# Optimization experiments

Measured on AMD Instinct MI355X. Metric: run time of the kernel, lower is better.

## Reference

```python
import jax, jax.numpy as jnp
import numpy as np

N_NODES = 100000
N_EDGES = 1600000
D_NODE = 32
D_EDGE = 16
D_HID = 64
D_OUT = 32


def setup_inputs() -> dict:
    key = jax.random.key(0)
    ks = jax.random.split(key, 7)
    x = jax.random.normal(ks[0], (N_NODES, D_NODE), dtype=jnp.float32)
    edge_index = jax.random.randint(ks[1], (2, N_EDGES), 0, N_NODES, dtype=jnp.int64)
    edge_attr = jax.random.normal(ks[2], (N_EDGES, D_EDGE), dtype=jnp.float32)
    # 2-layer MLP params (Linear -> ReLU -> Linear), He-ish scaling
    W1 = jax.random.normal(ks[3], (D_NODE + D_EDGE, D_HID), dtype=jnp.float32) * (2.0 / (D_NODE + D_EDGE)) ** 0.5
    b1 = jnp.zeros((D_HID,), dtype=jnp.float32)
    W2 = jax.random.normal(ks[4], (D_HID, D_OUT), dtype=jnp.float32) * (2.0 / D_HID) ** 0.5
    b2 = jnp.zeros((D_OUT,), dtype=jnp.float32)
    return {"x": x, "edge_index": edge_index, "edge_attr": edge_attr,
            "W1": W1, "b1": b1, "W2": W2, "b2": b2}


def reference(x, edge_index, edge_attr, W1, b1, W2, b2):
    row, col = edge_index[0], edge_index[1]
    # gather source-node feats and concat with edge feats: [E, d_node + d_edge]
    inp = jnp.concatenate([x[col], edge_attr], axis=1)
    # 2-layer MLP over edges
    h = jax.nn.relu(inp @ W1 + b1)
    messages = h @ W2 + b2  # [E, d_out]
    # scatter-sum aggregate by destination node
    message = jax.ops.segment_sum(messages, row, num_segments=x.shape[0])
    return message
```

## Files before the change

kernel.cpp:

```cpp
#include <hip/hip_runtime.h>
#include <hip/hip_bf16.h>
#include <stdint.h>

#define N_NODES 100000
#define N_EDGES 1600000
#define D_NODE  32
#define D_EDGE  16
#define D_IN    48
#define D_HID   64
#define D_OUT   32

#define NFLAGS_OFF  ((size_t)0)
#define NB1_OFF     ((size_t)64)
#define NB2_OFF     ((size_t)320)
#define W1BF_OFF    ((size_t)1024)
#define W2BF_OFF    ((size_t)9216)
#define COUNTS_OFF  ((size_t)65536)
#define OFFSETS_OFF ((size_t)466944)
#define BLKSUM_OFF  ((size_t)917504)
#define RANK_OFF    ((size_t)1048576)
#define MSG_OFF     ((size_t)8388608)

#define SCAN_NB 391

typedef __attribute__((ext_vector_type(8))) short bf16x8;
typedef __attribute__((ext_vector_type(4))) float f32x4;

__device__ inline float bf2f(unsigned int u16) {
    return __uint_as_float(u16 << 16);
}
__device__ inline unsigned short f2bf_rne(float f) {
    unsigned int x = __float_as_uint(f);
    unsigned int r = (x + 0x7FFFu + ((x >> 16) & 1u)) >> 16;
    return (unsigned short)r;
}
__device__ inline unsigned int pk_bf2(float a, float b) {
    float2 f; f.x = a; f.y = b;
    __hip_bfloat162 h = __float22bfloat162_rn(f);
    return *reinterpret_cast<unsigned int*>(&h);
}
__device__ inline float ld_f(const void* p, int i, int isbf) {
    if (isbf) return bf2f(((const unsigned short*)p)[i]);
    return ((const float*)p)[i];
}
__device__ inline bf16x8 pack_bf8(float4 v0, float4 v1) {
    union { unsigned int u[4]; bf16x8 v; } r;
    r.u[0] = pk_bf2(v0.x, v0.y);
    r.u[1] = pk_bf2(v0.z, v0.w);
    r.u[2] = pk_bf2(v1.x, v1.y);
    r.u[3] = pk_bf2(v1.z, v1.w);
    return r.v;
}

__global__ __launch_bounds__(256) void prep_kernel(
        const void* __restrict__ xq, const void* __restrict__ idxq,
        const void* __restrict__ W1q, const void* __restrict__ b1q,
        const void* __restrict__ W2q, const void* __restrict__ b2q,
        char* __restrict__ ws) {
    const int t = threadIdx.x;
    const int i0 = blockIdx.x * 256 + t;
    int* counts = (int*)(ws + COUNTS_OFF);
    if (i0 < N_NODES) counts[i0] = 0;
    if (blockIdx.x != 0) return;

    __shared__ int s_isbf;
    if (t < 64) {
        unsigned short u = ((const unsigned short*)xq)[t];
        unsigned long long mb = __ballot(((u >> 7) & 0xFF) >= 140);
        int wodd = ((const int*)idxq)[2 * t + 1];
        unsigned long long mi = __ballot(wodd != 0);
        if (t == 0) {
            int* flags = (int*)(ws + NFLAGS_OFF);
            flags[0] = (mb == 0ULL);
            flags[1] = (mi == 0ULL);
            s_isbf = (mb == 0ULL);
        }
    }
    __syncthreads();
    const int isbf = s_isbf;
    float* b1 = (float*)(ws + NB1_OFF);
    float* b2 = (float*)(ws + NB2_OFF);
    unsigned short* w1b = (unsigned short*)(ws + W1BF_OFF);
    unsigned short* w2b = (unsigned short*)(ws + W2BF_OFF);

    if (t < D_HID) b1[t] = ld_f(b1q, t, isbf);
    if (t < D_OUT) b2[t] = ld_f(b2q, t, isbf);

    for (int i = t; i < D_HID * 64; i += 256) {
        int n = i >> 6, k = i & 63;
        float v = (k < D_IN) ? ld_f(W1q, k * D_HID + n, isbf) : 0.0f;
        w1b[i] = f2bf_rne(v);
    }
    for (int i = t; i < D_OUT * 64; i += 256) {
        int n = i >> 6, k = i & 63;
        w2b[i] = f2bf_rne(ld_f(W2q, k * D_OUT + n, isbf));
    }
}

__global__ __launch_bounds__(256) void hist_kernel(const void* __restrict__ idxq,
                                                   char* __restrict__ ws,
                                                   int* __restrict__ rankb) {
    const int is64 = ((const int*)(ws + NFLAGS_OFF))[1];
    const int e = blockIdx.x * 256 + threadIdx.x;
    int dst;
    if (is64) dst = (int)((const long long*)idxq)[e];
    else      dst = ((const int*)idxq)[e];
    rankb[e] = atomicAdd((int*)(ws + COUNTS_OFF) + dst, 1);
}

__global__ __launch_bounds__(256) void scan_block_kernel(char* __restrict__ ws) {
    __shared__ int s[256];
    const int* counts = (const int*)(ws + COUNTS_OFF);
    int* offs   = (int*)(ws + OFFSETS_OFF);
    int* blksum = (int*)(ws + BLKSUM_OFF);
    const int t = threadIdx.x;
    const int i = blockIdx.x * 256 + t;
    int v = (i < N_NODES) ? counts[i] : 0;
    s[t] = v;
    __syncthreads();
    for (int d = 1; d < 256; d <<= 1) {
        int a = (t >= d) ? s[t - d] : 0;
        __syncthreads();
        s[t] += a;
        __syncthreads();
    }
    if (i < N_NODES) offs[i] = s[t] - v;
    if (t == 255) blksum[blockIdx.x] = s[255];
}

__global__ __launch_bounds__(256) void scan_add_kernel(char* __restrict__ ws) {
    __shared__ int s[256];
    int* offs = (int*)(ws + OFFSETS_OFF);
    const int* blksum = (const int*)(ws + BLKSUM_OFF);
    const int t = threadIdx.x;
    const int b = blockIdx.x;
    int acc = 0;
    for (int j = t; j < b; j += 256) acc += blksum[j];
    s[t] = acc;
    __syncthreads();
    for (int d = 128; d > 0; d >>= 1) {
        if (t < d) s[t] += s[t + d];
        __syncthreads();
    }
    const int prefix = s[0];
    const int i = b * 256 + t;
    if (i < N_NODES) offs[i] += prefix;
    if (i == 0) offs[N_NODES] = N_EDGES;
}

__global__ __launch_bounds__(256) void edge_mlp_mfma_kernel(
        const void* __restrict__ xq,
        const void* __restrict__ idxq,
        const void* __restrict__ eaq,
        const char* __restrict__ wsro,
        const int* __restrict__ rankb,
        unsigned short* __restrict__ msg) {
    const int isbf = ((const int*)(wsro + NFLAGS_OFF))[0];
    const int is64 = ((const int*)(wsro + NFLAGS_OFF))[1];

    __shared__ __align__(16) unsigned short hbuf[4][16][72];

    const int w   = threadIdx.x >> 6;
    const int l   = threadIdx.x & 63;
    const int m16 = l & 15;
    const int q   = l >> 4;

    const unsigned short* w1b = (const unsigned short*)(wsro + W1BF_OFF);
    const unsigned short* w2b = (const unsigned short*)(wsro + W2BF_OFF);
    const float* b1 = (const float*)(wsro + NB1_OFF);
    const float* b2 = (const float*)(wsro + NB2_OFF);
    const int* offs = (const int*)(wsro + OFFSETS_OFF);

    bf16x8 w1f[4][2], w2f[2][2];
#pragma unroll
    for (int t = 0; t < 4; ++t)
#pragma unroll
        for (int c = 0; c < 2; ++c)
            w1f[t][c] = *(const bf16x8*)(w1b + ((t * 16 + m16) * 64 + c * 32 + q * 8));
#pragma unroll
    for (int t = 0; t < 2; ++t)
#pragma unroll
        for (int c = 0; c < 2; ++c)
            w2f[t][c] = *(const bf16x8*)(w2b + ((t * 16 + m16) * 64 + c * 32 + q * 8));

    const int eb = blockIdx.x * 256 + w * 64;

    int srcv[4], posv[4];
#pragma unroll
    for (int g = 0; g < 4; ++g) {
        const int e = eb + g * 16 + m16;
        int dst;
        if (is64) {
            const long long* ip = (const long long*)idxq;
            dst = (int)ip[e];
            srcv[g] = (int)ip[N_EDGES + e];
        } else {
            const int* ip = (const int*)idxq;
            dst = ip[e];
            srcv[g] = ip[N_EDGES + e];
        }
        posv[g] = offs[dst] + rankb[e];
    }

    const float b1v[4] = { b1[m16], b1[16 + m16], b1[32 + m16], b1[48 + m16] };
    const float b2v[2] = { b2[m16], b2[16 + m16] };
    const int mrow = l >> 2;
    const int sub  = l & 3;

    auto loadA = [&](int g, bf16x8& a0, bf16x8& a1) {
        const int e = eb + g * 16 + m16;
        if (isbf) {
            const unsigned short* x  = (const unsigned short*)xq;
            const unsigned short* ea = (const unsigned short*)eaq;
            a0 = *(const bf16x8*)(x + (size_t)srcv[g] * D_NODE + q * 8);
            a1 = *(const bf16x8*)(ea + (size_t)e * D_EDGE + (q & 1) * 8);
        } else {
            const float* x  = (const float*)xq;
            const float* ea = (const float*)eaq;
            const float4* xp = (const float4*)(x + (size_t)srcv[g] * D_NODE + q * 8);
            a0 = pack_bf8(xp[0], xp[1]);
            const float4* ap = (const float4*)(ea + (size_t)e * D_EDGE + (q & 1) * 8);
            a1 = pack_bf8(ap[0], ap[1]);
        }
    };

    bf16x8 A0c, A1c, A0n, A1n;
    loadA(0, A0c, A1c);

#pragma unroll 1
    for (int g = 0; g < 4; ++g) {
        if (g < 3) loadA(g + 1, A0n, A1n);

#pragma unroll
        for (int t = 0; t < 4; ++t) {
            f32x4 c;
            c[0] = c[1] = c[2] = c[3] = b1v[t];
            c = __builtin_amdgcn_mfma_f32_16x16x32_bf16(A0c, w1f[t][0], c, 0, 0, 0);
            c = __builtin_amdgcn_mfma_f32_16x16x32_bf16(A1c, w1f[t][1], c, 0, 0, 0);
            unsigned int u0 = pk_bf2(fmaxf(c[0], 0.0f), fmaxf(c[1], 0.0f));
            unsigned int u1 = pk_bf2(fmaxf(c[2], 0.0f), fmaxf(c[3], 0.0f));
            hbuf[w][q * 4 + 0][t * 16 + m16] = (unsigned short)u0;
            hbuf[w][q * 4 + 1][t * 16 + m16] = (unsigned short)(u0 >> 16);
            hbuf[w][q * 4 + 2][t * 16 + m16] = (unsigned short)u1;
            hbuf[w][q * 4 + 3][t * 16 + m16] = (unsigned short)(u1 >> 16);
        }

        bf16x8 a20 = *(const bf16x8*)(&hbuf[w][m16][q * 8]);
        bf16x8 a21 = *(const bf16x8*)(&hbuf[w][m16][32 + q * 8]);
#pragma unroll
        for (int t = 0; t < 2; ++t) {
            f32x4 c;
            c[0] = c[1] = c[2] = c[3] = b2v[t];
            c = __builtin_amdgcn_mfma_f32_16x16x32_bf16(a20, w2f[t][0], c, 0, 0, 0);
            c = __builtin_amdgcn_mfma_f32_16x16x32_bf16(a21, w2f[t][1], c, 0, 0, 0);
            unsigned int u0 = pk_bf2(c[0], c[1]);
            unsigned int u1 = pk_bf2(c[2], c[3]);
            hbuf[w][q * 4 + 0][t * 16 + m16] = (unsigned short)u0;
            hbuf[w][q * 4 + 1][t * 16 + m16] = (unsigned short)(u0 >> 16);
            hbuf[w][q * 4 + 2][t * 16 + m16] = (unsigned short)u1;
            hbuf[w][q * 4 + 3][t * 16 + m16] = (unsigned short)(u1 >> 16);
        }

        const int posm = __shfl(posv[g], mrow, 64);
        uint4 rowv = *(const uint4*)(&hbuf[w][mrow][sub * 8]);
        *(uint4*)(msg + (size_t)posm * D_OUT + sub * 8) = rowv;

        A0c = A0n; A1c = A1n;
    }
}

__global__ __launch_bounds__(256) void reduce_kernel(
        const char* __restrict__ wsro, const unsigned short* __restrict__ msg,
        void* __restrict__ out) {
    const int isbf = ((const int*)(wsro + NFLAGS_OFF))[0];
    const int* offs = (const int*)(wsro + OFFSETS_OFF);
    const int node = (blockIdx.x * 256 + threadIdx.x) >> 6;
    if (node >= N_NODES) return;
    const int l   = threadIdx.x & 63;
    const int r   = l >> 2;
    const int sub = l & 3;

    const int lo = offs[node], hi = offs[node + 1];
    float a0 = 0.f, a1 = 0.f, a2 = 0.f, a3 = 0.f,
          a4 = 0.f, a5 = 0.f, a6 = 0.f, a7 = 0.f;
    for (int k = lo; k < hi; k += 16) {
        const int row = k + r;
        if (row < hi) {
            uint4 v = *(const uint4*)(msg + (size_t)row * D_OUT + sub * 8);
            a0 += __uint_as_float(v.x << 16); a1 += __uint_as_float(v.x & 0xFFFF0000u);
            a2 += __uint_as_float(v.y << 16); a3 += __uint_as_float(v.y & 0xFFFF0000u);
            a4 += __uint_as_float(v.z << 16); a5 += __uint_as_float(v.z & 0xFFFF0000u);
            a6 += __uint_as_float(v.w << 16); a7 += __uint_as_float(v.w & 0xFFFF0000u);
        }
    }
#pragma unroll
    for (int mask = 4; mask <= 32; mask <<= 1) {
        a0 += __shfl_xor(a0, mask, 64); a1 += __shfl_xor(a1, mask, 64);
        a2 += __shfl_xor(a2, mask, 64); a3 += __shfl_xor(a3, mask, 64);
        a4 += __shfl_xor(a4, mask, 64); a5 += __shfl_xor(a5, mask, 64);
        a6 += __shfl_xor(a6, mask, 64); a7 += __shfl_xor(a7, mask, 64);
    }
    if (r == 0) {
        if (isbf) {
            uint4 p;
            p.x = pk_bf2(a0, a1); p.y = pk_bf2(a2, a3);
            p.z = pk_bf2(a4, a5); p.w = pk_bf2(a6, a7);
            *(uint4*)((unsigned short*)out + (size_t)node * D_OUT + sub * 8) = p;
        } else {
            float4* op = (float4*)((float*)out + (size_t)node * D_OUT + sub * 8);
            float4 v0; v0.x = a0; v0.y = a1; v0.z = a2; v0.w = a3;
            float4 v1; v1.x = a4; v1.y = a5; v1.z = a6; v1.w = a7;
            op[0] = v0;
            op[1] = v1;
        }
    }
}

extern "C" void kernel_launch(void* const* d_in, const int* in_sizes, int n_in,
                              void* d_out, int out_size, void* d_ws, size_t ws_size,
                              hipStream_t stream) {
    const void* x   = d_in[0];
    const void* idx = d_in[1];
    const void* ea  = d_in[2];
    const void* W1  = d_in[3];
    const void* b1  = d_in[4];
    const void* W2  = d_in[5];
    const void* b2  = d_in[6];
    char* ws = (char*)d_ws;

    hipLaunchKernelGGL(prep_kernel, dim3(SCAN_NB), dim3(256), 0, stream,
                       x, idx, W1, b1, W2, b2, ws);

    hipLaunchKernelGGL(hist_kernel, dim3(N_EDGES / 256), dim3(256), 0, stream,
                       idx, ws, (int*)(ws + RANK_OFF));

    hipLaunchKernelGGL(scan_block_kernel, dim3(SCAN_NB), dim3(256), 0, stream, ws);
    hipLaunchKernelGGL(scan_add_kernel,   dim3(SCAN_NB), dim3(256), 0, stream, ws);

    hipLaunchKernelGGL(edge_mlp_mfma_kernel, dim3(N_EDGES / 256), dim3(256), 0, stream,
                       x, idx, ea, (const char*)ws,
                       (const int*)(ws + RANK_OFF), (unsigned short*)(ws + MSG_OFF));

    hipLaunchKernelGGL(reduce_kernel, dim3((N_NODES + 3) / 4), dim3(256), 0, stream,
                       (const char*)ws, (const unsigned short*)(ws + MSG_OFF), d_out);
}
```

Measured before the change: 384.4 us.

## Fuse edge MLP with per-node reduction after permuting edges into destination order

Edge sources and edge attributes (converted to bf16) are permuted into destination-sorted order by a new kernel. A fused per-node kernel then runs the MFMA MLP over each node's edge segment and accumulates the output in registers, replacing the separate message write and reduce pass. x is pre-converted to bf16 in the prep kernel, and the b2 bias is folded in as degree times b2. This removes the bf16 message buffer round trip but adds a scatter pass, and each wave now handles a node with about 16 edges, so padding waste and tail lanes may cost MFMA efficiency.

```diff
diff --git a/kernel.cpp b/kernel.cpp
--- a/kernel.cpp
+++ b/kernel.cpp
@@ -15,13 +15,18 @@
 #define NB2_OFF     ((size_t)320)
 #define W1BF_OFF    ((size_t)1024)
 #define W2BF_OFF    ((size_t)9216)
-#define COUNTS_OFF  ((size_t)65536)
-#define OFFSETS_OFF ((size_t)466944)
-#define BLKSUM_OFF  ((size_t)917504)
-#define RANK_OFF    ((size_t)1048576)
-#define MSG_OFF     ((size_t)8388608)
-
-#define SCAN_NB 391
+#define XB_OFF      ((size_t)16384)
+#define COUNTS_OFF  ((size_t)6416384)
+#define OFFS_OFF    ((size_t)6816384)
+#define BLKSUM_OFF  ((size_t)7216640)
+#define RANK_OFF    ((size_t)7218688)
+#define SRCS_OFF    ((size_t)13618688)
+#define EASORT_OFF  ((size_t)20018688)
+
+#define SCAN_NB  391
+#define PREP_NB  1563
+#define EDGE_NB  6250
+#define FUSED_NB 25000
 
 typedef __attribute__((ext_vector_type(8))) short bf16x8;
 typedef __attribute__((ext_vector_type(4))) float f32x4;
@@ -43,13 +48,11 @@
     if (isbf) return bf2f(((const unsigned short*)p)[i]);
     return ((const float*)p)[i];
 }
-__device__ inline bf16x8 pack_bf8(float4 v0, float4 v1) {
-    union { unsigned int u[4]; bf16x8 v; } r;
-    r.u[0] = pk_bf2(v0.x, v0.y);
-    r.u[1] = pk_bf2(v0.z, v0.w);
-    r.u[2] = pk_bf2(v1.x, v1.y);
-    r.u[3] = pk_bf2(v1.z, v1.w);
-    return r.v;
+__device__ inline uint4 pack8(float4 v0, float4 v1) {
+    uint4 r;
+    r.x = pk_bf2(v0.x, v0.y); r.y = pk_bf2(v0.z, v0.w);
+    r.z = pk_bf2(v1.x, v1.y); r.w = pk_bf2(v1.z, v1.w);
+    return r;
 }
 
 __global__ __launch_bounds__(256) void prep_kernel(
@@ -58,26 +61,39 @@
         const void* __restrict__ W2q, const void* __restrict__ b2q,
         char* __restrict__ ws) {
     const int t = threadIdx.x;
-    const int i0 = blockIdx.x * 256 + t;
-    int* counts = (int*)(ws + COUNTS_OFF);
-    if (i0 < N_NODES) counts[i0] = 0;
-    if (blockIdx.x != 0) return;
-
     __shared__ int s_isbf;
     if (t < 64) {
         unsigned short u = ((const unsigned short*)xq)[t];
         unsigned long long mb = __ballot(((u >> 7) & 0xFF) >= 140);
-        int wodd = ((const int*)idxq)[2 * t + 1];
-        unsigned long long mi = __ballot(wodd != 0);
-        if (t == 0) {
-            int* flags = (int*)(ws + NFLAGS_OFF);
-            flags[0] = (mb == 0ULL);
-            flags[1] = (mi == 0ULL);
-            s_isbf = (mb == 0ULL);
+        if (t == 0) s_isbf = (mb == 0ULL);
+        if (blockIdx.x == 0) {
+            int wodd = ((const int*)idxq)[2 * t + 1];
+            unsigned long long mi = __ballot(wodd != 0);
+            if (t == 0) {
+                int* flags = (int*)(ws + NFLAGS_OFF);
+                flags[0] = (mb == 0ULL);
+                flags[1] = (mi == 0ULL);
+            }
         }
     }
     __syncthreads();
     const int isbf = s_isbf;
+
+    const int i0 = blockIdx.x * 256 + t;
+    if (i0 < N_NODES) ((int*)(ws + COUNTS_OFF))[i0] = 0;
+
+    const int g8 = i0 * 8;
+    if (g8 < N_NODES * D_NODE) {
+        unsigned short* xb = (unsigned short*)(ws + XB_OFF);
+        if (isbf) {
+            *(uint4*)(xb + g8) = *(const uint4*)((const unsigned short*)xq + g8);
+        } else {
+            const float4* xp = (const float4*)((const float*)xq + g8);
+            *(uint4*)(xb + g8) = pack8(xp[0], xp[1]);
+        }
+    }
+
+    if (blockIdx.x != 0) return;
     float* b1 = (float*)(ws + NB1_OFF);
     float* b2 = (float*)(ws + NB2_OFF);
     unsigned short* w1b = (unsigned short*)(ws + W1BF_OFF);
@@ -111,7 +127,7 @@
 __global__ __launch_bounds__(256) void scan_block_kernel(char* __restrict__ ws) {
     __shared__ int s[256];
     const int* counts = (const int*)(ws + COUNTS_OFF);
-    int* offs   = (int*)(ws + OFFSETS_OFF);
+    int* offs   = (int*)(ws + OFFS_OFF);
     int* blksum = (int*)(ws + BLKSUM_OFF);
     const int t = threadIdx.x;
     const int i = blockIdx.x * 256 + t;
@@ -130,7 +146,7 @@
 
 __global__ __launch_bounds__(256) void scan_add_kernel(char* __restrict__ ws) {
     __shared__ int s[256];
-    int* offs = (int*)(ws + OFFSETS_OFF);
+    int* offs = (int*)(ws + OFFS_OFF);
     const int* blksum = (const int*)(ws + BLKSUM_OFF);
     const int t = threadIdx.x;
     const int b = blockIdx.x;
@@ -148,15 +164,48 @@
     if (i == 0) offs[N_NODES] = N_EDGES;
 }
 
-__global__ __launch_bounds__(256) void edge_mlp_mfma_kernel(
-        const void* __restrict__ xq,
-        const void* __restrict__ idxq,
-        const void* __restrict__ eaq,
+__global__ __launch_bounds__(256) void permute_kernel(
+        const void* __restrict__ idxq, const void* __restrict__ eaq,
         const char* __restrict__ wsro,
         const int* __restrict__ rankb,
-        unsigned short* __restrict__ msg) {
+        int* __restrict__ srcsort, unsigned short* __restrict__ easort) {
     const int isbf = ((const int*)(wsro + NFLAGS_OFF))[0];
     const int is64 = ((const int*)(wsro + NFLAGS_OFF))[1];
+    const int* offs = (const int*)(wsro + OFFS_OFF);
+    const int e = blockIdx.x * 256 + threadIdx.x;
+    int dst, src;
+    if (is64) {
+        const long long* ip = (const long long*)idxq;
+        dst = (int)ip[e];
+        src = (int)ip[N_EDGES + e];
+    } else {
+        const int* ip = (const int*)idxq;
+        dst = ip[e];
+        src = ip[N_EDGES + e];
+    }
+    const int pos = offs[dst] + rankb[e];
+
+    uint4 p0, p1;
+    if (isbf) {
+        const uint4* ap = (const uint4*)((const unsigned short*)eaq + (size_t)e * D_EDGE);
+        p0 = ap[0]; p1 = ap[1];
+    } else {
+        const float4* ap = (const float4*)((const float*)eaq + (size_t)e * D_EDGE);
+        p0 = pack8(ap[0], ap[1]);
+        p1 = pack8(ap[2], ap[3]);
+    }
+    uint4* row = (uint4*)(easort + (size_t)pos * D_EDGE);
+    row[0] = p0;
+    row[1] = p1;
+    srcsort[pos] = src;
+}
+
+__global__ __launch_bounds__(256) void fused_node_kernel(
+        const char* __restrict__ wsro,
+        const int* __restrict__ srcsort,
+        const unsigned short* __restrict__ easort,
+        void* __restrict__ out) {
+    const int isbf = ((const int*)(wsro + NFLAGS_OFF))[0];
 
     __shared__ __align__(16) unsigned short hbuf[4][16][72];
 
@@ -167,9 +216,10 @@
 
     const unsigned short* w1b = (const unsigned short*)(wsro + W1BF_OFF);
     const unsigned short* w2b = (const unsigned short*)(wsro + W2BF_OFF);
+    const unsigned short* xb  = (const unsigned short*)(wsro + XB_OFF);
     const float* b1 = (const float*)(wsro + NB1_OFF);
     const float* b2 = (const float*)(wsro + NB2_OFF);
-    const int* offs = (const int*)(wsro + OFFSETS_OFF);
+    const int* offs = (const int*)(wsro + OFFS_OFF);
 
     bf16x8 w1f[4][2], w2f[2][2];
 #pragma unroll
@@ -183,60 +233,31 @@
         for (int c = 0; c < 2; ++c)
             w2f[t][c] = *(const bf16x8*)(w2b + ((t * 16 + m16) * 64 + c * 32 + q * 8));
 
-    const int eb = blockIdx.x * 256 + w * 64;
-
-    int srcv[4], posv[4];
-#pragma unroll
-    for (int g = 0; g < 4; ++g) {
-        const int e = eb + g * 16 + m16;
-        int dst;
-        if (is64) {
-            const long long* ip = (const long long*)idxq;
-            dst = (int)ip[e];
-            srcv[g] = (int)ip[N_EDGES + e];
-        } else {
-            const int* ip = (const int*)idxq;
-            dst = ip[e];
-            srcv[g] = ip[N_EDGES + e];
-        }
-        posv[g] = offs[dst] + rankb[e];
-    }
+    const int n = blockIdx.x * 4 + w;
+    const int lo = offs[n], hi = offs[n + 1];
+    const int deg = hi - lo;
 
     const float b1v[4] = { b1[m16], b1[16 + m16], b1[32 + m16], b1[48 + m16] };
-    const float b2v[2] = { b2[m16], b2[16 + m16] };
-    const int mrow = l >> 2;
-    const int sub  = l & 3;
-
-    auto loadA = [&](int g, bf16x8& a0, bf16x8& a1) {
-        const int e = eb + g * 16 + m16;
-        if (isbf) {
-            const unsigned short* x  = (const unsigned short*)xq;
-            const unsigned short* ea = (const unsigned short*)eaq;
-            a0 = *(const bf16x8*)(x + (size_t)srcv[g] * D_NODE + q * 8);
-            a1 = *(const bf16x8*)(ea + (size_t)e * D_EDGE + (q & 1) * 8);
-        } else {
-            const float* x  = (const float*)xq;
-            const float* ea = (const float*)eaq;
-            const float4* xp = (const float4*)(x + (size_t)srcv[g] * D_NODE + q * 8);
-            a0 = pack_bf8(xp[0], xp[1]);
-            const float4* ap = (const float4*)(ea + (size_t)e * D_EDGE + (q & 1) * 8);
-            a1 = pack_bf8(ap[0], ap[1]);
-        }
-    };
-
-    bf16x8 A0c, A1c, A0n, A1n;
-    loadA(0, A0c, A1c);
-
-#pragma unroll 1
-    for (int g = 0; g < 4; ++g) {
-        if (g < 3) loadA(g + 1, A0n, A1n);
+
+    f32x4 acc0, acc1;
+    acc0[0]=acc0[1]=acc0[2]=acc0[3]=0.f;
+    acc1[0]=acc1[1]=acc1[2]=acc1[3]=0.f;
+    float s0 = 0.f, s1 = 0.f;
+
+    for (int base = lo; base < hi; base += 16) {
+        const int slot = base + m16;
+        const int sidx = (slot < N_EDGES) ? slot : (N_EDGES - 1);
+        const int src  = srcsort[sidx];
+
+        bf16x8 a0 = *(const bf16x8*)(xb + (size_t)src * D_NODE + q * 8);
+        bf16x8 a1 = *(const bf16x8*)(easort + (size_t)sidx * D_EDGE + (q & 1) * 8);
 
 #pragma unroll
         for (int t = 0; t < 4; ++t) {
             f32x4 c;
             c[0] = c[1] = c[2] = c[3] = b1v[t];
-            c = __builtin_amdgcn_mfma_f32_16x16x32_bf16(A0c, w1f[t][0], c, 0, 0, 0);
-            c = __builtin_amdgcn_mfma_f32_16x16x32_bf16(A1c, w1f[t][1], c, 0, 0, 0);
+            c = __builtin_amdgcn_mfma_f32_16x16x32_bf16(a0, w1f[t][0], c, 0, 0, 0);
+            c = __builtin_amdgcn_mfma_f32_16x16x32_bf16(a1, w1f[t][1], c, 0, 0, 0);
             unsigned int u0 = pk_bf2(fmaxf(c[0], 0.0f), fmaxf(c[1], 0.0f));
             unsigned int u1 = pk_bf2(fmaxf(c[2], 0.0f), fmaxf(c[3], 0.0f));
             hbuf[w][q * 4 + 0][t * 16 + m16] = (unsigned short)u0;
@@ -247,72 +268,42 @@
 
         bf16x8 a20 = *(const bf16x8*)(&hbuf[w][m16][q * 8]);
         bf16x8 a21 = *(const bf16x8*)(&hbuf[w][m16][32 + q * 8]);
-#pragma unroll
-        for (int t = 0; t < 2; ++t) {
-            f32x4 c;
-            c[0] = c[1] = c[2] = c[3] = b2v[t];
-            c = __builtin_amdgcn_mfma_f32_16x16x32_bf16(a20, w2f[t][0], c, 0, 0, 0);
-            c = __builtin_amdgcn_mfma_f32_16x16x32_bf16(a21, w2f[t][1], c, 0, 0, 0);
-            unsigned int u0 = pk_bf2(c[0], c[1]);
-            unsigned int u1 = pk_bf2(c[2], c[3]);
-            hbuf[w][q * 4 + 0][t * 16 + m16] = (unsigned short)u0;
-            hbuf[w][q * 4 + 1][t * 16 + m16] = (unsigned short)(u0 >> 16);
-            hbuf[w][q * 4 + 2][t * 16 + m16] = (unsigned short)u1;
-            hbuf[w][q * 4 + 3][t * 16 + m16] = (unsigned short)(u1 >> 16);
+        f32x4 c0, c1;
+        c0[0]=c0[1]=c0[2]=c0[3]=0.f;
+        c1[0]=c1[1]=c1[2]=c1[3]=0.f;
+        c0 = __builtin_amdgcn_mfma_f32_16x16x32_bf16(a20, w2f[0][0], c0, 0, 0, 0);
+        c0 = __builtin_amdgcn_mfma_f32_16x16x32_bf16(a21, w2f[0][1], c0, 0, 0, 0);
+        c1 = __builtin_amdgcn_mfma_f32_16x16x32_bf16(a20, w2f[1][0], c1, 0, 0, 0);
+        c1 = __builtin_amdgcn_mfma_f32_16x16x32_bf16(a21, w2f[1][1], c1, 0, 0, 0);
+
+        const int rem = hi - base;
+        if (rem >= 16) {
+#pragma unroll
+            for (int r = 0; r < 4; ++r) { acc0[r] += c0[r]; acc1[r] += c1[r]; }
+        } else {
+#pragma unroll
+            for (int r = 0; r < 4; ++r) {
+                if (q * 4 + r < rem) { acc0[r] += c0[r]; acc1[r] += c1[r]; }
+            }
         }
-
-        const int posm = __shfl(posv[g], mrow, 64);
-        uint4 rowv = *(const uint4*)(&hbuf[w][mrow][sub * 8]);
-        *(uint4*)(msg + (size_t)posm * D_OUT + sub * 8) = rowv;
-
-        A0c = A0n; A1c = A1n;
-    }
-}
-
-__global__ __launch_bounds__(256) void reduce_kernel(
-        const char* __restrict__ wsro, const unsigned short* __restrict__ msg,
-        void* __restrict__ out) {
-    const int isbf = ((const int*)(wsro + NFLAGS_OFF))[0];
-    const int* offs = (const int*)(wsro + OFFSETS_OFF);
-    const int node = (blockIdx.x * 256 + threadIdx.x) >> 6;
-    if (node >= N_NODES) return;
-    const int l   = threadIdx.x & 63;
-    const int r   = l >> 2;
-    const int sub = l & 3;
-
-    const int lo = offs[node], hi = offs[node + 1];
-    float a0 = 0.f, a1 = 0.f, a2 = 0.f, a3 = 0.f,
-          a4 = 0.f, a5 = 0.f, a6 = 0.f, a7 = 0.f;
-    for (int k = lo; k < hi; k += 16) {
-        const int row = k + r;
-        if (row < hi) {
-            uint4 v = *(const uint4*)(msg + (size_t)row * D_OUT + sub * 8);
-            a0 += __uint_as_float(v.x << 16); a1 += __uint_as_float(v.x & 0xFFFF0000u);
-            a2 += __uint_as_float(v.y << 16); a3 += __uint_as_float(v.y & 0xFFFF0000u);
-            a4 += __uint_as_float(v.z << 16); a5 += __uint_as_float(v.z & 0xFFFF0000u);
-            a6 += __uint_as_float(v.w << 16); a7 += __uint_as_float(v.w & 0xFFFF0000u);
-        }
-    }
-#pragma unroll
-    for (int mask = 4; mask <= 32; mask <<= 1) {
-        a0 += __shfl_xor(a0, mask, 64); a1 += __shfl_xor(a1, mask, 64);
-        a2 += __shfl_xor(a2, mask, 64); a3 += __shfl_xor(a3, mask, 64);
-        a4 += __shfl_xor(a4, mask, 64); a5 += __shfl_xor(a5, mask, 64);
-        a6 += __shfl_xor(a6, mask, 64); a7 += __shfl_xor(a7, mask, 64);
-    }
-    if (r == 0) {
-        if (isbf) {
-            uint4 p;
-            p.x = pk_bf2(a0, a1); p.y = pk_bf2(a2, a3);
-            p.z = pk_bf2(a4, a5); p.w = pk_bf2(a6, a7);
-            *(uint4*)((unsigned short*)out + (size_t)node * D_OUT + sub * 8) = p;
-        } else {
-            float4* op = (float4*)((float*)out + (size_t)node * D_OUT + sub * 8);
-            float4 v0; v0.x = a0; v0.y = a1; v0.z = a2; v0.w = a3;
-            float4 v1; v1.x = a4; v1.y = a5; v1.z = a6; v1.w = a7;
-            op[0] = v0;
-            op[1] = v1;
-        }
+    }
+
+    s0 = acc0[0] + acc0[1] + acc0[2] + acc0[3];
+    s1 = acc1[0] + acc1[1] + acc1[2] + acc1[3];
+    s0 += __shfl_xor(s0, 16, 64);  s1 += __shfl_xor(s1, 16, 64);
+    s0 += __shfl_xor(s0, 32, 64);  s1 += __shfl_xor(s1, 32, 64);
+
+    s0 += (float)deg * b2[m16];
+    s1 += (float)deg * b2[16 + m16];
+
+    if (isbf) {
+        unsigned short* o16 = (unsigned short*)out + (size_t)n * D_OUT;
+        if (q == 0) o16[m16]      = f2bf_rne(s0);
+        else if (q == 1) o16[16 + m16] = f2bf_rne(s1);
+    } else {
+        float* of = (float*)out + (size_t)n * D_OUT;
+        if (q == 0) of[m16]      = s0;
+        else if (q == 1) of[16 + m16] = s1;
     }
 }
 
@@ -328,19 +319,20 @@
     const void* b2  = d_in[6];
     char* ws = (char*)d_ws;
 
-    hipLaunchKernelGGL(prep_kernel, dim3(SCAN_NB), dim3(256), 0, stream,
+    hipLaunchKernelGGL(prep_kernel, dim3(PREP_NB), dim3(256), 0, stream,
                        x, idx, W1, b1, W2, b2, ws);
 
-    hipLaunchKernelGGL(hist_kernel, dim3(N_EDGES / 256), dim3(256), 0, stream,
+    hipLaunchKernelGGL(hist_kernel, dim3(EDGE_NB), dim3(256), 0, stream,
                        idx, ws, (int*)(ws + RANK_OFF));
 
     hipLaunchKernelGGL(scan_block_kernel, dim3(SCAN_NB), dim3(256), 0, stream, ws);
     hipLaunchKernelGGL(scan_add_kernel,   dim3(SCAN_NB), dim3(256), 0, stream, ws);
 
-    hipLaunchKernelGGL(edge_mlp_mfma_kernel, dim3(N_EDGES / 256), dim3(256), 0, stream,
-                       x, idx, ea, (const char*)ws,
-                       (const int*)(ws + RANK_OFF), (unsigned short*)(ws + MSG_OFF));
-
-    hipLaunchKernelGGL(reduce_kernel, dim3((N_NODES + 3) / 4), dim3(256), 0, stream,
-                       (const char*)ws, (const unsigned short*)(ws + MSG_OFF), d_out);
-}
+    hipLaunchKernelGGL(permute_kernel, dim3(EDGE_NB), dim3(256), 0, stream,
+                       idx, ea, (const char*)ws, (const int*)(ws + RANK_OFF),
+                       (int*)(ws + SRCS_OFF), (unsigned short*)(ws + EASORT_OFF));
+
+    hipLaunchKernelGGL(fused_node_kernel, dim3(FUSED_NB), dim3(256), 0, stream,
+                       (const char*)ws, (const int*)(ws + SRCS_OFF),
+                       (const unsigned short*)(ws + EASORT_OFF), d_out);
+}
```

Result: slower. 501.8 us (+30.6%).
